# Performance work log

Measured on AMD Instinct MI355X. Metric: run time of the kernel, lower is better.

Reference implementation:

```python
import jax, jax.numpy as jnp
import numpy as np

N = 16384
IMRATIO = 0.0732
MARGIN = 1.0


def setup_inputs() -> dict:
    key = jax.random.key(0)
    k1, k2 = jax.random.split(key)
    preds = jax.random.normal(k1, (N,), dtype=jnp.float32)
    targets = (jax.random.uniform(k2, (N,)) < IMRATIO).astype(jnp.int32)
    return {"preds": preds, "targets": targets}


def reference(preds, targets):
    # positive = preds[targets==1]; negative = preds[targets==0]
    # loss = mean over P x N pairs of (1 - (p_i - n_j))**2 + margin * relu(1 - (p_i - n_j))
    # Expressed jit-compatibly as a mask-weighted full pairwise reduction (same math).
    pos_w = (targets == 1).astype(preds.dtype)  # [N]
    neg_w = (targets == 0).astype(preds.dtype)  # [N]
    one_minus_diff = 1.0 - (preds[:, None] - preds[None, :])  # [N, N]
    vals = one_minus_diff * one_minus_diff + MARGIN * jax.nn.relu(one_minus_diff)
    w = pos_w[:, None] * neg_w[None, :]  # [N, N] pair indicator
    num_pairs = pos_w.sum() * neg_w.sum()
    return (vals * w).sum() / num_pairs
```

## Files before the change

kernel.cpp:

```cpp
#include <hip/hip_runtime.h>


#define NSEG  64
#define MAXP  4096

__device__ __forceinline__ double wave_reduce_f64(double v) {
    #pragma unroll
    for (int off = 32; off > 0; off >>= 1) v += __shfl_xor(v, off, 64);
    return v;
}

__device__ __forceinline__ float wave_reduce_f32(float v) {
    #pragma unroll
    for (int off = 32; off > 0; off >>= 1) v += __shfl_xor(v, off, 64);
    return v;
}

__global__ __launch_bounds__(256)
void aucm_scan(const float* __restrict__ preds,
               const int* __restrict__ tgt,
               int n,
               double* __restrict__ momPart,
               int* __restrict__ cnt,
               float* __restrict__ posSeg) {
    __shared__ float sPos[256];
    __shared__ int sCnt;
    __shared__ double sRed[4][4];

    const int tid = threadIdx.x;
    const int b   = blockIdx.x;
    const int wave = tid >> 6;
    if (tid == 0) sCnt = 0;
    __syncthreads();

    const int i = b * 256 + tid;
    float a = 0.f, a2 = 0.f, nv = 0.f, n2 = 0.f;
    if (i < n) {
        const float p = preds[i];
        if (tgt[i] == 1) {
            const float av = 1.0f - p;
            a = av; a2 = av * av;
            const int idx = atomicAdd(&sCnt, 1);
            sPos[idx] = av;
        } else {
            nv = p; n2 = p * p;
        }
    }
    __syncthreads();
    const int c = sCnt;
    if (tid < c) posSeg[b * 256 + tid] = sPos[tid];

    const float rA  = wave_reduce_f32(a);
    const float rA2 = wave_reduce_f32(a2);
    const float rN  = wave_reduce_f32(nv);
    const float rN2 = wave_reduce_f32(n2);
    if ((tid & 63) == 0) {
        sRed[wave][0] = (double)rA;  sRed[wave][1] = (double)rA2;
        sRed[wave][2] = (double)rN;  sRed[wave][3] = (double)rN2;
    }
    __syncthreads();
    if (tid == 0) {
        double t0 = 0, t1 = 0, t2 = 0, t3 = 0;
        #pragma unroll
        for (int w = 0; w < 4; ++w) {
            t0 += sRed[w][0]; t1 += sRed[w][1];
            t2 += sRed[w][2]; t3 += sRed[w][3];
        }
        momPart[b * 4 + 0] = t0; momPart[b * 4 + 1] = t1;
        momPart[b * 4 + 2] = t2; momPart[b * 4 + 3] = t3;
        cnt[b] = c;
    }
}

__global__ __launch_bounds__(256)
void aucm_relu(const float* __restrict__ preds,
               const int* __restrict__ tgt,
               int n,
               const int* __restrict__ cnt,
               const float* __restrict__ posSeg,
               double* __restrict__ reluPart) {
    __shared__ int pref[NSEG + 1];
    __shared__ float sA[MAXP];
    __shared__ double sRed[4];

    const int tid   = threadIdx.x;
    const int jb    = blockIdx.x & 63;
    const int slice = blockIdx.x >> 6;

    if (tid == 0) {
        int run = 0;
        for (int s = 0; s < NSEG; ++s) { pref[s] = run; run += cnt[s]; }
        pref[NSEG] = run;
    }
    __syncthreads();

    const int total = pref[NSEG];
    const int per   = (total + 3) >> 2;
    const int lo    = slice * per;
    const int hi    = min(total, lo + per);
    const int cntS  = max(0, hi - lo);

    for (int s = tid; s < cntS; s += 256) {
        const int g = lo + s;
        int l = 0, h = NSEG;
        while (h - l > 1) { const int m = (l + h) >> 1; if (pref[m] <= g) l = m; else h = m; }
        sA[s] = posSeg[l * 256 + (g - pref[l])];
    }
    __syncthreads();

    const int j = jb * 256 + tid;
    float acc = 0.f;
    if (j < n && tgt[j] == 0) {
        const float pj = preds[j];
        int k = 0;
        for (; k + 8 <= cntS; k += 8) {
            #pragma unroll
            for (int u = 0; u < 8; ++u)
                acc += fmaxf(sA[k + u] + pj, 0.f);
        }
        for (; k < cntS; ++k) acc += fmaxf(sA[k] + pj, 0.f);
    }

    double r = wave_reduce_f64((double)acc);
    if ((tid & 63) == 0) sRed[tid >> 6] = r;
    __syncthreads();
    if (tid == 0)
        reluPart[blockIdx.x] = sRed[0] + sRed[1] + sRed[2] + sRed[3];
}

__global__ __launch_bounds__(256)
void aucm_fin(const double* __restrict__ momPart,
              const int* __restrict__ cnt,
              const double* __restrict__ reluPart,
              int nRelu, int n,
              float* __restrict__ out, float margin) {
    __shared__ double sRed[4][6];
    const int tid = threadIdx.x;
    const int wave = tid >> 6;

    double mA = 0, mA2 = 0, mN = 0, mN2 = 0, r = 0, pc = 0;
    for (int i = tid; i < NSEG; i += 256) {
        mA  += momPart[i * 4 + 0]; mA2 += momPart[i * 4 + 1];
        mN  += momPart[i * 4 + 2]; mN2 += momPart[i * 4 + 3];
        pc  += (double)cnt[i];
    }
    for (int i = tid; i < nRelu; i += 256) r += reluPart[i];

    mA = wave_reduce_f64(mA);  mA2 = wave_reduce_f64(mA2);
    mN = wave_reduce_f64(mN);  mN2 = wave_reduce_f64(mN2);
    r  = wave_reduce_f64(r);   pc  = wave_reduce_f64(pc);
    if ((tid & 63) == 0) {
        sRed[wave][0] = mA; sRed[wave][1] = mA2; sRed[wave][2] = mN;
        sRed[wave][3] = mN2; sRed[wave][4] = r;  sRed[wave][5] = pc;
    }
    __syncthreads();
    if (tid == 0) {
        double tA = 0, tA2 = 0, tN = 0, tN2 = 0, tR = 0, tP = 0;
        #pragma unroll
        for (int w = 0; w < 4; ++w) {
            tA += sRed[w][0]; tA2 += sRed[w][1]; tN += sRed[w][2];
            tN2 += sRed[w][3]; tR += sRed[w][4]; tP += sRed[w][5];
        }
        const double P  = tP;
        const double Nn = (double)n - tP;
        const double sq = Nn * tA2 + 2.0 * tA * tN + P * tN2;
        out[0] = (float)((sq + (double)margin * tR) / (P * Nn));
    }
}

extern "C" void kernel_launch(void* const* d_in, const int* in_sizes, int n_in,
                              void* d_out, int out_size, void* d_ws, size_t ws_size,
                              hipStream_t stream) {
    const float* preds = (const float*)d_in[0];
    const int*   tgt   = (const int*)d_in[1];
    float* out = (float*)d_out;
    const int n = in_sizes[0];

    char* ws = (char*)d_ws;
    double* momPart  = (double*)(ws + 0);
    int*    cnt      = (int*)(ws + 2048);
    double* reluPart = (double*)(ws + 2304);
    float*  posSeg   = (float*)(ws + 4352);

    aucm_scan<<<NSEG, 256, 0, stream>>>(preds, tgt, n, momPart, cnt, posSeg);
    aucm_relu<<<NSEG * 4, 256, 0, stream>>>(preds, tgt, n, cnt, posSeg, reluPart);
    aucm_fin<<<1, 256, 0, stream>>>(momPart, cnt, reluPart, NSEG * 4, n, out,
                                    1.0f );
}
```

Measured before the change: 67.10 us.

## Fuse scan, relu and finalize kernels into one cooperative kernel with grid syncs

Replaces the three launches (scan, pairwise relu, finalize) with one cooperative kernel of 256 blocks that uses grid.sync between phases. The scan phase now uses 64-element segments handled by a single wave, with ballot and popcount compaction instead of shared atomics. The compaction of positives into shared memory uses a parallel prefix scan over the per-segment counts instead of a serial prefix plus binary search. The aim is to remove launch gaps and serial setup work, at the cost of grid-wide barriers and a serial per-thread copy loop over each segment.

```diff
diff --git a/kernel.cpp b/kernel.cpp
--- a/kernel.cpp
+++ b/kernel.cpp
@@ -1,8 +1,12 @@
 #include <hip/hip_runtime.h>
+#include <hip/hip_cooperative_groups.h>
+
+namespace cg = cooperative_groups;
 
 
-#define NSEG  64
-#define MAXP  4096
+#define NBLK 256
+#define SEG  64
+#define MAXS 4096
 
 __device__ __forceinline__ double wave_reduce_f64(double v) {
     #pragma unroll
@@ -17,98 +21,81 @@
 }
 
 __global__ __launch_bounds__(256)
-void aucm_scan(const float* __restrict__ preds,
+void aucm_coop(const float* __restrict__ preds,
                const int* __restrict__ tgt,
                int n,
                double* __restrict__ momPart,
                int* __restrict__ cnt,
-               float* __restrict__ posSeg) {
-    __shared__ float sPos[256];
-    __shared__ int sCnt;
-    __shared__ double sRed[4][4];
+               double* __restrict__ reluPart,
+               float* __restrict__ posSeg,
+               float* __restrict__ out,
+               float margin) {
+    cg::grid_group grid = cg::this_grid();
 
-    const int tid = threadIdx.x;
-    const int b   = blockIdx.x;
+    __shared__ float sList[MAXS];
+    __shared__ int   sWaveSum[4];
+    __shared__ double sRed[4][6];
+
+    const int tid  = threadIdx.x;
+    const int lane = tid & 63;
     const int wave = tid >> 6;
-    if (tid == 0) sCnt = 0;
-    __syncthreads();
+    const int b    = blockIdx.x;
 
-    const int i = b * 256 + tid;
-    float a = 0.f, a2 = 0.f, nv = 0.f, n2 = 0.f;
-    if (i < n) {
-        const float p = preds[i];
-        if (tgt[i] == 1) {
-            const float av = 1.0f - p;
-            a = av; a2 = av * av;
-            const int idx = atomicAdd(&sCnt, 1);
-            sPos[idx] = av;
-        } else {
-            nv = p; n2 = p * p;
+    if (wave == 0) {
+        const int i = b * SEG + lane;
+        float p = 0.f; int t = 0;
+        if (i < n) { p = preds[i]; t = tgt[i]; }
+        const bool isPos = (i < n) && (t == 1);
+        const float av = 1.0f - p;
+        const unsigned long long mask = __ballot(isPos);
+        const int pfx = __popcll(mask & ((1ull << lane) - 1ull));
+        if (isPos) posSeg[b * SEG + pfx] = av;
+
+        float a  = isPos ? av : 0.f;
+        float a2 = isPos ? av * av : 0.f;
+        float nv = (!isPos && i < n) ? p : 0.f;
+        float n2 = (!isPos && i < n) ? p * p : 0.f;
+        const float rA  = wave_reduce_f32(a);
+        const float rA2 = wave_reduce_f32(a2);
+        const float rN  = wave_reduce_f32(nv);
+        const float rN2 = wave_reduce_f32(n2);
+        if (lane == 0) {
+            momPart[b * 4 + 0] = (double)rA;
+            momPart[b * 4 + 1] = (double)rA2;
+            momPart[b * 4 + 2] = (double)rN;
+            momPart[b * 4 + 3] = (double)rN2;
+            cnt[b] = __popcll(mask);
         }
     }
+    grid.sync();
+
+    const int c = cnt[tid];
+    int v = c;
+    #pragma unroll
+    for (int off = 1; off < 64; off <<= 1) {
+        const int u = __shfl_up(v, off, 64);
+        if (lane >= off) v += u;
+    }
+    if (lane == 63) sWaveSum[wave] = v;
     __syncthreads();
-    const int c = sCnt;
-    if (tid < c) posSeg[b * 256 + tid] = sPos[tid];
+    int waveBase = 0;
+    #pragma unroll
+    for (int w = 0; w < 4; ++w) if (w < wave) waveBase += sWaveSum[w];
+    const int excl  = waveBase + v - c;
+    const int total = sWaveSum[0] + sWaveSum[1] + sWaveSum[2] + sWaveSum[3];
 
-    const float rA  = wave_reduce_f32(a);
-    const float rA2 = wave_reduce_f32(a2);
-    const float rN  = wave_reduce_f32(nv);
-    const float rN2 = wave_reduce_f32(n2);
-    if ((tid & 63) == 0) {
-        sRed[wave][0] = (double)rA;  sRed[wave][1] = (double)rA2;
-        sRed[wave][2] = (double)rN;  sRed[wave][3] = (double)rN2;
-    }
-    __syncthreads();
-    if (tid == 0) {
-        double t0 = 0, t1 = 0, t2 = 0, t3 = 0;
-        #pragma unroll
-        for (int w = 0; w < 4; ++w) {
-            t0 += sRed[w][0]; t1 += sRed[w][1];
-            t2 += sRed[w][2]; t3 += sRed[w][3];
-        }
-        momPart[b * 4 + 0] = t0; momPart[b * 4 + 1] = t1;
-        momPart[b * 4 + 2] = t2; momPart[b * 4 + 3] = t3;
-        cnt[b] = c;
-    }
-}
-
-__global__ __launch_bounds__(256)
-void aucm_relu(const float* __restrict__ preds,
-               const int* __restrict__ tgt,
-               int n,
-               const int* __restrict__ cnt,
-               const float* __restrict__ posSeg,
-               double* __restrict__ reluPart) {
-    __shared__ int pref[NSEG + 1];
-    __shared__ float sA[MAXP];
-    __shared__ double sRed[4];
-
-    const int tid   = threadIdx.x;
-    const int jb    = blockIdx.x & 63;
-    const int slice = blockIdx.x >> 6;
-
-    if (tid == 0) {
-        int run = 0;
-        for (int s = 0; s < NSEG; ++s) { pref[s] = run; run += cnt[s]; }
-        pref[NSEG] = run;
-    }
-    __syncthreads();
-
-    const int total = pref[NSEG];
+    const int slice = b >> 6;
     const int per   = (total + 3) >> 2;
     const int lo    = slice * per;
     const int hi    = min(total, lo + per);
     const int cntS  = max(0, hi - lo);
-
-    for (int s = tid; s < cntS; s += 256) {
-        const int g = lo + s;
-        int l = 0, h = NSEG;
-        while (h - l > 1) { const int m = (l + h) >> 1; if (pref[m] <= g) l = m; else h = m; }
-        sA[s] = posSeg[l * 256 + (g - pref[l])];
+    for (int k = 0; k < c; ++k) {
+        const int g = excl + k;
+        if (g >= lo && g < hi) sList[g - lo] = posSeg[tid * SEG + k];
     }
     __syncthreads();
 
-    const int j = jb * 256 + tid;
+    const int j = (b & 63) * 256 + tid;
     float acc = 0.f;
     if (j < n && tgt[j] == 0) {
         const float pj = preds[j];
@@ -116,55 +103,45 @@
         for (; k + 8 <= cntS; k += 8) {
             #pragma unroll
             for (int u = 0; u < 8; ++u)
-                acc += fmaxf(sA[k + u] + pj, 0.f);
+                acc += fmaxf(sList[k + u] + pj, 0.f);
         }
-        for (; k < cntS; ++k) acc += fmaxf(sA[k] + pj, 0.f);
+        for (; k < cntS; ++k) acc += fmaxf(sList[k] + pj, 0.f);
     }
-
     double r = wave_reduce_f64((double)acc);
-    if ((tid & 63) == 0) sRed[tid >> 6] = r;
+    if (lane == 0) sRed[wave][0] = r;
     __syncthreads();
     if (tid == 0)
-        reluPart[blockIdx.x] = sRed[0] + sRed[1] + sRed[2] + sRed[3];
-}
+        reluPart[b] = sRed[0][0] + sRed[1][0] + sRed[2][0] + sRed[3][0];
+    grid.sync();
 
-__global__ __launch_bounds__(256)
-void aucm_fin(const double* __restrict__ momPart,
-              const int* __restrict__ cnt,
-              const double* __restrict__ reluPart,
-              int nRelu, int n,
-              float* __restrict__ out, float margin) {
-    __shared__ double sRed[4][6];
-    const int tid = threadIdx.x;
-    const int wave = tid >> 6;
-
-    double mA = 0, mA2 = 0, mN = 0, mN2 = 0, r = 0, pc = 0;
-    for (int i = tid; i < NSEG; i += 256) {
-        mA  += momPart[i * 4 + 0]; mA2 += momPart[i * 4 + 1];
-        mN  += momPart[i * 4 + 2]; mN2 += momPart[i * 4 + 3];
-        pc  += (double)cnt[i];
-    }
-    for (int i = tid; i < nRelu; i += 256) r += reluPart[i];
-
-    mA = wave_reduce_f64(mA);  mA2 = wave_reduce_f64(mA2);
-    mN = wave_reduce_f64(mN);  mN2 = wave_reduce_f64(mN2);
-    r  = wave_reduce_f64(r);   pc  = wave_reduce_f64(pc);
-    if ((tid & 63) == 0) {
-        sRed[wave][0] = mA; sRed[wave][1] = mA2; sRed[wave][2] = mN;
-        sRed[wave][3] = mN2; sRed[wave][4] = r;  sRed[wave][5] = pc;
-    }
-    __syncthreads();
-    if (tid == 0) {
-        double tA = 0, tA2 = 0, tN = 0, tN2 = 0, tR = 0, tP = 0;
-        #pragma unroll
-        for (int w = 0; w < 4; ++w) {
-            tA += sRed[w][0]; tA2 += sRed[w][1]; tN += sRed[w][2];
-            tN2 += sRed[w][3]; tR += sRed[w][4]; tP += sRed[w][5];
+    if (b == 0) {
+        double mA = 0, mA2 = 0, mN = 0, mN2 = 0, rr = 0, pc = 0;
+        mA  = momPart[tid * 4 + 0];
+        mA2 = momPart[tid * 4 + 1];
+        mN  = momPart[tid * 4 + 2];
+        mN2 = momPart[tid * 4 + 3];
+        rr  = reluPart[tid];
+        pc  = (double)cnt[tid];
+        mA = wave_reduce_f64(mA);  mA2 = wave_reduce_f64(mA2);
+        mN = wave_reduce_f64(mN);  mN2 = wave_reduce_f64(mN2);
+        rr = wave_reduce_f64(rr);  pc  = wave_reduce_f64(pc);
+        if (lane == 0) {
+            sRed[wave][0] = mA; sRed[wave][1] = mA2; sRed[wave][2] = mN;
+            sRed[wave][3] = mN2; sRed[wave][4] = rr; sRed[wave][5] = pc;
         }
-        const double P  = tP;
-        const double Nn = (double)n - tP;
-        const double sq = Nn * tA2 + 2.0 * tA * tN + P * tN2;
-        out[0] = (float)((sq + (double)margin * tR) / (P * Nn));
+        __syncthreads();
+        if (tid == 0) {
+            double tA = 0, tA2 = 0, tN = 0, tN2 = 0, tR = 0, tP = 0;
+            #pragma unroll
+            for (int w = 0; w < 4; ++w) {
+                tA += sRed[w][0]; tA2 += sRed[w][1]; tN += sRed[w][2];
+                tN2 += sRed[w][3]; tR += sRed[w][4]; tP += sRed[w][5];
+            }
+            const double P  = tP;
+            const double Nn = (double)n - tP;
+            const double sq = Nn * tA2 + 2.0 * tA * tN + P * tN2;
+            out[0] = (float)((sq + (double)margin * tR) / (P * Nn));
+        }
     }
 }
 
@@ -174,16 +151,18 @@
     const float* preds = (const float*)d_in[0];
     const int*   tgt   = (const int*)d_in[1];
     float* out = (float*)d_out;
-    const int n = in_sizes[0];
+    int n = in_sizes[0];
 
     char* ws = (char*)d_ws;
     double* momPart  = (double*)(ws + 0);
-    int*    cnt      = (int*)(ws + 2048);
-    double* reluPart = (double*)(ws + 2304);
-    float*  posSeg   = (float*)(ws + 4352);
+    int*    cnt      = (int*)(ws + 8192);
+    double* reluPart = (double*)(ws + 9216);
+    float*  posSeg   = (float*)(ws + 11264);
+    float margin = 1.0f;
 
-    aucm_scan<<<NSEG, 256, 0, stream>>>(preds, tgt, n, momPart, cnt, posSeg);
-    aucm_relu<<<NSEG * 4, 256, 0, stream>>>(preds, tgt, n, cnt, posSeg, reluPart);
-    aucm_fin<<<1, 256, 0, stream>>>(momPart, cnt, reluPart, NSEG * 4, n, out,
-                                    1.0f );
+    void* args[] = { (void*)&preds, (void*)&tgt, (void*)&n,
+                     (void*)&momPart, (void*)&cnt, (void*)&reluPart,
+                     (void*)&posSeg, (void*)&out, (void*)&margin };
+    hipLaunchCooperativeKernel((void*)aucm_coop, dim3(NBLK), dim3(256),
+                               args, 0, stream);
 }
```

Measured after the change: 120.0 us. +78.8%, slower.
